# Performance work log

Hardware: AMD Instinct MI355X
Metric: run time of the kernel (lower is better)

Reference implementation:

```python
import jax, jax.numpy as jnp
import numpy as np

SIGMA = 1.0
NUM_CLASSES = 10


def setup_inputs() -> dict:
    key = jax.random.key(0)
    k1, k2, k3, k4 = jax.random.split(key, 4)
    ns, nt, d = 4096, 4096, 256
    return {
        "source_feature": jax.random.normal(k1, (ns, d), dtype=jnp.float32),
        "source_label": jax.random.randint(k2, (ns,), 0, NUM_CLASSES),
        "target_feature": jax.random.normal(k3, (nt, d), dtype=jnp.float32),
        "class_weight": jax.random.uniform(k4, (NUM_CLASSES,), dtype=jnp.float32),
    }


def _rbf_gram(x, y, sigma):
    # K[i, j] = exp(-||x_i - y_j||^2 / (2*sigma)); [n, m]
    x2 = jnp.sum(x * x, axis=-1)  # [n]
    y2 = jnp.sum(y * y, axis=-1)  # [m]
    sq = x2[:, None] + y2[None, :] - 2.0 * (x @ y.T)
    sq = jnp.maximum(sq, 0.0)
    return jnp.exp(-sq / (2.0 * sigma))


def reference(source_feature, source_label, target_feature, class_weight):
    ns = source_feature.shape[0]
    nt = target_feature.shape[0]
    w = class_weight[source_label]          # [ns] per-sample weight
    n = jnp.sum(w)                          # weighted source count

    Kss = _rbf_gram(source_feature, source_feature, SIGMA)  # [ns, ns]
    Ktt = _rbf_gram(target_feature, target_feature, SIGMA)  # [nt, nt]
    Kst = _rbf_gram(source_feature, target_feature, SIGMA)  # [ns, nt]

    first = jnp.einsum('i,ij,j->', w, Kss, w)
    sec = jnp.sum(Ktt)
    third = jnp.einsum('i,ij->', w, Kst)

    return first / (n * n) + sec / (nt * nt) - 2.0 * third / (n * nt)
```

## Files before the change

kernel.cpp:

```cpp
#include <hip/hip_runtime.h>
#include <hip/hip_bf16.h>


typedef float f32x4 __attribute__((ext_vector_type(4)));

#define D 256

static __device__ __forceinline__ unsigned char f32_to_e4m3(float f) {
    unsigned int u = __float_as_uint(f);
    unsigned int sg = (u >> 24) & 0x80;
    unsigned int um = u & 0x7FFFFFFF;
    unsigned int r = um + 0x0007FFFF + ((um >> 20) & 1);
    int e8 = (int)((r >> 23) & 0xFF) - 127 + 7;
    unsigned int m8 = (r >> 20) & 7;
    if (e8 <= 0) return (unsigned char)sg;
    if (e8 > 15 || (e8 == 15 && m8 == 7))
        return (unsigned char)(sg | 0x7E);
    return (unsigned char)(sg | ((unsigned)e8 << 3) | m8);
}


__global__ __launch_bounds__(256) void prep_kernel(
    const float* __restrict__ sf, const float* __restrict__ tf,
    const int* __restrict__ lbl, const float* __restrict__ cw,
    unsigned char* __restrict__ sfb, unsigned char* __restrict__ tfb,
    float* __restrict__ x2s, float* __restrict__ x2t,
    float* __restrict__ wv, int ns)
{
    int row = blockIdx.x * 4 + (threadIdx.x >> 6);
    int t = threadIdx.x & 63;
    bool is_src = row < ns;
    int r = is_src ? row : row - ns;
    const float* src = (is_src ? sf : tf) + (size_t)r * D;
    unsigned char* dstb = is_src ? sfb : tfb;

    float4 v = ((const float4*)src)[t];
    uchar4 q;
    q.x = f32_to_e4m3(v.x); q.y = f32_to_e4m3(v.y);
    q.z = f32_to_e4m3(v.z); q.w = f32_to_e4m3(v.w);

    int g = r >> 4, rr = r & 15;
    int s_ = t >> 3;
    int kg = (t >> 1) & 3;
    int j0 = (t & 1) * 4;
    size_t idx = ((size_t)(g * 8 + s_) * 512) + (size_t)(rr + 16 * kg) * 8 + j0;
    *(uchar4*)(dstb + idx) = q;

    float s = v.x * v.x + v.y * v.y + v.z * v.z + v.w * v.w;
    #pragma unroll
    for (int o = 32; o; o >>= 1) s += __shfl_xor(s, o);

    if (t == 0) {
        if (is_src) { wv[r] = cw[lbl[r]]; x2s[r] = s; }
        else        { x2t[r] = s; }
    }
}

__global__ __launch_bounds__(256, 3) void gram_kernel(
    const unsigned char* __restrict__ sfb, const unsigned char* __restrict__ tfb,
    const float* __restrict__ x2s, const float* __restrict__ x2t,
    const float* __restrict__ wv, float* __restrict__ bout,
    int ti_s, int ti_t)
{
    int tri_s = ti_s * (ti_s + 1) / 2;
    int tri_t = ti_t * (ti_t + 1) / 2;
    int blk = blockIdx.x;

    int mode, bi, bj;
    const unsigned char *X, *Y;
    const float *x2xp, *x2yp;
    if (blk < tri_s + tri_t) {
        int T, idx;
        if (blk < tri_s) { mode = 0; idx = blk; T = ti_s; X = sfb; Y = sfb; x2xp = x2s; x2yp = x2s; }
        else { mode = 1; idx = blk - tri_s; T = ti_t; X = tfb; Y = tfb; x2xp = x2t; x2yp = x2t; }
        bi = (int)((2.0f * T + 1.0f -
                    sqrtf((float)((2 * T + 1) * (2 * T + 1) - 8 * idx))) * 0.5f);
        if (bi < 0) bi = 0;
        if (bi > T - 1) bi = T - 1;
        int base = bi * (2 * T - bi + 1) / 2;
        while (base > idx) { --bi; base = bi * (2 * T - bi + 1) / 2; }
        while (idx >= base + (T - bi)) { base += (T - bi); ++bi; }
        bj = bi + (idx - base);
    } else {
        int idx = blk - tri_s - tri_t;
        mode = 2; bi = idx / ti_t; bj = idx % ti_t;
        X = sfb; Y = tfb; x2xp = x2s; x2yp = x2t;
    }
    float factor = (mode != 2 && bi != bj) ? 2.0f : 1.0f;

    int wid = threadIdx.x >> 6;
    int lane = threadIdx.x & 63;
    int wr = wid >> 1, wc = wid & 1;
    int R0 = bi * 128 + wr * 64;
    int C0 = bj * 128 + wc * 64;

    const unsigned char* XA = X + (size_t)(R0 >> 4) * 4096 + lane * 8;
    const unsigned char* YB = Y + (size_t)(C0 >> 4) * 4096 + lane * 8;

    f32x4 acc[4][4] = {};
    long af[2][4], bf_[2][4];
    #pragma unroll
    for (int m = 0; m < 4; ++m) {
        af[0][m]  = *(const long*)(XA + (size_t)(m * 8) * 512);
        bf_[0][m] = *(const long*)(YB + (size_t)(m * 8) * 512);
    }
    #pragma unroll
    for (int s = 0; s < 8; ++s) {
        const int cur = s & 1, nxt = cur ^ 1;
        if (s < 7) {
            #pragma unroll
            for (int m = 0; m < 4; ++m) {
                af[nxt][m]  = *(const long*)(XA + (size_t)(m * 8 + s + 1) * 512);
                bf_[nxt][m] = *(const long*)(YB + (size_t)(m * 8 + s + 1) * 512);
            }
        }
        #pragma unroll
        for (int m = 0; m < 4; ++m)
            #pragma unroll
            for (int n = 0; n < 4; ++n)
                acc[m][n] = __builtin_amdgcn_mfma_f32_16x16x32_fp8_fp8(
                    af[cur][m], bf_[cur][n], acc[m][n], 0, 0, 0);
    }

    int crow = (lane >> 4) * 4;
    int ccol = lane & 15;
    float s = 0.0f;
    #pragma unroll
    for (int m = 0; m < 4; ++m) {
        #pragma unroll
        for (int r = 0; r < 4; ++r) {
            int gr = R0 + 16 * m + crow + r;
            float rx2 = x2xp[gr];
            float rw = (mode != 1) ? wv[gr] : 1.0f;
            #pragma unroll
            for (int n = 0; n < 4; ++n) {
                int gc = C0 + 16 * n + ccol;
                float S = acc[m][n][r];
                float sq = fmaxf(x2yp[gc] + rx2 - 2.0f * S, 0.0f);
                float K = __expf(-0.5f * sq);
                if (mode != 2 && gr == gc) K = 1.0f;
                float wf = (mode == 0) ? rw * wv[gc] : rw;
                s += wf * K;
            }
        }
    }
    s *= factor;
    #pragma unroll
    for (int o = 32; o; o >>= 1) s += __shfl_xor(s, o);

    __shared__ float bsum[4];
    if (lane == 0) bsum[wid] = s;
    __syncthreads();
    if (threadIdx.x == 0)
        bout[blk] = (bsum[0] + bsum[1]) + (bsum[2] + bsum[3]);
}

__global__ __launch_bounds__(1024) void reduce_kernel(
    const float* __restrict__ wv, int ns,
    const float* __restrict__ bout, int tri_s, int tri_t, int nb,
    float* __restrict__ out, int nt)
{
    int tid = threadIdx.x;
    float n = 0.0f, a0 = 0.0f, a1 = 0.0f, a2 = 0.0f;
    for (int i = tid; i < ns; i += 1024) n += wv[i];
    for (int i = tid; i < nb; i += 1024) {
        float v = bout[i];
        if (i < tri_s) a0 += v;
        else if (i < tri_s + tri_t) a1 += v;
        else a2 += v;
    }
    #pragma unroll
    for (int o = 32; o; o >>= 1) {
        n  += __shfl_xor(n, o);
        a0 += __shfl_xor(a0, o);
        a1 += __shfl_xor(a1, o);
        a2 += __shfl_xor(a2, o);
    }
    __shared__ float ln[16], l0[16], l1[16], l2[16];
    int w = tid >> 6;
    if ((tid & 63) == 0) { ln[w] = n; l0[w] = a0; l1[w] = a1; l2[w] = a2; }
    __syncthreads();
    if (tid == 0) {
        float N = 0, A0 = 0, A1 = 0, A2 = 0;
        #pragma unroll
        for (int i = 0; i < 16; ++i) { N += ln[i]; A0 += l0[i]; A1 += l1[i]; A2 += l2[i]; }
        float fnt = (float)nt;
        out[0] = A0 / (N * N) + A1 / (fnt * fnt) - 2.0f * A2 / (N * fnt);
    }
}

extern "C" void kernel_launch(void* const* d_in, const int* in_sizes, int n_in,
                              void* d_out, int out_size, void* d_ws, size_t ws_size,
                              hipStream_t stream) {
    const float* sf = (const float*)d_in[0];
    const int* lbl = (const int*)d_in[1];
    const float* tf = (const float*)d_in[2];
    const float* cw = (const float*)d_in[3];
    float* out = (float*)d_out;

    int ns = in_sizes[1];
    int d = in_sizes[0] / ns;
    int nt = in_sizes[2] / d;

    char* p = (char*)d_ws;
    unsigned char* sfb = (unsigned char*)p;  p += (size_t)ns * d;
    unsigned char* tfb = (unsigned char*)p;  p += (size_t)nt * d;
    float* x2s = (float*)p;                  p += (size_t)ns * sizeof(float);
    float* x2t = (float*)p;                  p += (size_t)nt * sizeof(float);
    float* wv  = (float*)p;                  p += (size_t)ns * sizeof(float);
    float* bout = (float*)p;

    prep_kernel<<<(ns + nt) / 4, 256, 0, stream>>>(sf, tf, lbl, cw, sfb, tfb,
                                                   x2s, x2t, wv, ns);

    int ti_s = ns / 128, ti_t = nt / 128;
    int tri_s = ti_s * (ti_s + 1) / 2;
    int tri_t = ti_t * (ti_t + 1) / 2;
    int nblocks = tri_s + tri_t + ti_s * ti_t;
    gram_kernel<<<nblocks, 256, 0, stream>>>(sfb, tfb, x2s, x2t, wv, bout,
                                             ti_s, ti_t);

    reduce_kernel<<<1, 1024, 0, stream>>>(wv, ns, bout, tri_s, tri_t, nblocks,
                                          out, nt);
}
```

Baseline: 46.31 us.

## Skip negligible RBF exponentials per row and deepen fp8 operand prefetch

The epilogue now computes the four squared distances for a row first. It skips the exp, weight loads and accumulation when every lane's minimum distance is at least 180, since exp(-90) underflows to roughly zero in float32. Diagonal terms are no longer set to 1 inside the tiles. They are zeroed there and added back analytically in the reduce kernel, as sum(w^2) for the source-source term and nt for the target-target term. The fragment prefetch is also deepened from double to quad buffering, loading three steps ahead, and the x2 column norms are hoisted out of the row loop. The deeper prefetch uses more registers, and the skip adds wave-wide branching.

New measurement: 41.76 us. -9.8%, faster.

```diff
diff --git a/kernel.cpp b/kernel.cpp
--- a/kernel.cpp
+++ b/kernel.cpp
@@ -98,20 +98,24 @@
     const unsigned char* YB = Y + (size_t)(C0 >> 4) * 4096 + lane * 8;
 
     f32x4 acc[4][4] = {};
-    long af[2][4], bf_[2][4];
-    #pragma unroll
-    for (int m = 0; m < 4; ++m) {
-        af[0][m]  = *(const long*)(XA + (size_t)(m * 8) * 512);
-        bf_[0][m] = *(const long*)(YB + (size_t)(m * 8) * 512);
+    long af[4][4], bf_[4][4];
+    #pragma unroll
+    for (int sp = 0; sp < 3; ++sp) {
+        #pragma unroll
+        for (int m = 0; m < 4; ++m) {
+            af[sp][m]  = *(const long*)(XA + (size_t)(m * 8 + sp) * 512);
+            bf_[sp][m] = *(const long*)(YB + (size_t)(m * 8 + sp) * 512);
+        }
     }
     #pragma unroll
     for (int s = 0; s < 8; ++s) {
-        const int cur = s & 1, nxt = cur ^ 1;
-        if (s < 7) {
+        const int cur = s & 3;
+        if (s < 5) {
+            const int pf = (s + 3) & 3;
             #pragma unroll
             for (int m = 0; m < 4; ++m) {
-                af[nxt][m]  = *(const long*)(XA + (size_t)(m * 8 + s + 1) * 512);
-                bf_[nxt][m] = *(const long*)(YB + (size_t)(m * 8 + s + 1) * 512);
+                af[pf][m]  = *(const long*)(XA + (size_t)(m * 8 + s + 3) * 512);
+                bf_[pf][m] = *(const long*)(YB + (size_t)(m * 8 + s + 3) * 512);
             }
         }
         #pragma unroll
@@ -124,6 +128,10 @@
 
     int crow = (lane >> 4) * 4;
     int ccol = lane & 15;
+    float x2yc[4];
+    #pragma unroll
+    for (int n = 0; n < 4; ++n) x2yc[n] = x2yp[C0 + 16 * n + ccol];
+
     float s = 0.0f;
     #pragma unroll
     for (int m = 0; m < 4; ++m) {
@@ -131,16 +139,22 @@
         for (int r = 0; r < 4; ++r) {
             int gr = R0 + 16 * m + crow + r;
             float rx2 = x2xp[gr];
-            float rw = (mode != 1) ? wv[gr] : 1.0f;
-            #pragma unroll
-            for (int n = 0; n < 4; ++n) {
-                int gc = C0 + 16 * n + ccol;
-                float S = acc[m][n][r];
-                float sq = fmaxf(x2yp[gc] + rx2 - 2.0f * S, 0.0f);
-                float K = __expf(-0.5f * sq);
-                if (mode != 2 && gr == gc) K = 1.0f;
-                float wf = (mode == 0) ? rw * wv[gc] : rw;
-                s += wf * K;
+            float sq0 = fmaxf(rx2 + x2yc[0] - 2.0f * acc[m][0][r], 0.0f);
+            float sq1 = fmaxf(rx2 + x2yc[1] - 2.0f * acc[m][1][r], 0.0f);
+            float sq2 = fmaxf(rx2 + x2yc[2] - 2.0f * acc[m][2][r], 0.0f);
+            float sq3 = fmaxf(rx2 + x2yc[3] - 2.0f * acc[m][3][r], 0.0f);
+            float mn = fminf(fminf(sq0, sq1), fminf(sq2, sq3));
+            if (__any(mn < 180.0f)) {
+                float rw = (mode != 1) ? wv[gr] : 1.0f;
+                float sqv[4] = {sq0, sq1, sq2, sq3};
+                #pragma unroll
+                for (int n = 0; n < 4; ++n) {
+                    int gc = C0 + 16 * n + ccol;
+                    float K = __expf(-0.5f * sqv[n]);
+                    if (mode != 2 && gr == gc) K = 0.0f;
+                    float wf = (mode == 0) ? rw * wv[gc] : rw;
+                    s += wf * K;
+                }
             }
         }
     }
@@ -161,8 +175,12 @@
     float* __restrict__ out, int nt)
 {
     int tid = threadIdx.x;
-    float n = 0.0f, a0 = 0.0f, a1 = 0.0f, a2 = 0.0f;
-    for (int i = tid; i < ns; i += 1024) n += wv[i];
+    float n = 0.0f, dsq = 0.0f, a0 = 0.0f, a1 = 0.0f, a2 = 0.0f;
+    for (int i = tid; i < ns; i += 1024) {
+        float w = wv[i];
+        n += w;
+        dsq += w * w;
+    }
     for (int i = tid; i < nb; i += 1024) {
         float v = bout[i];
         if (i < tri_s) a0 += v;
@@ -171,21 +189,25 @@
     }
     #pragma unroll
     for (int o = 32; o; o >>= 1) {
-        n  += __shfl_xor(n, o);
-        a0 += __shfl_xor(a0, o);
-        a1 += __shfl_xor(a1, o);
-        a2 += __shfl_xor(a2, o);
-    }
-    __shared__ float ln[16], l0[16], l1[16], l2[16];
+        n   += __shfl_xor(n, o);
+        dsq += __shfl_xor(dsq, o);
+        a0  += __shfl_xor(a0, o);
+        a1  += __shfl_xor(a1, o);
+        a2  += __shfl_xor(a2, o);
+    }
+    __shared__ float ln[16], ld[16], l0[16], l1[16], l2[16];
     int w = tid >> 6;
-    if ((tid & 63) == 0) { ln[w] = n; l0[w] = a0; l1[w] = a1; l2[w] = a2; }
+    if ((tid & 63) == 0) { ln[w] = n; ld[w] = dsq; l0[w] = a0; l1[w] = a1; l2[w] = a2; }
     __syncthreads();
     if (tid == 0) {
-        float N = 0, A0 = 0, A1 = 0, A2 = 0;
-        #pragma unroll
-        for (int i = 0; i < 16; ++i) { N += ln[i]; A0 += l0[i]; A1 += l1[i]; A2 += l2[i]; }
+        float N = 0, DQ = 0, A0 = 0, A1 = 0, A2 = 0;
+        #pragma unroll
+        for (int i = 0; i < 16; ++i) {
+            N += ln[i]; DQ += ld[i]; A0 += l0[i]; A1 += l1[i]; A2 += l2[i];
+        }
         float fnt = (float)nt;
-        out[0] = A0 / (N * N) + A1 / (fnt * fnt) - 2.0f * A2 / (N * fnt);
+        out[0] = (A0 + DQ) / (N * N) + (A1 + fnt) / (fnt * fnt)
+               - 2.0f * A2 / (N * fnt);
     }
 }
 
```
